# Kernel tuning notes

Hardware: AMD Instinct MI355X
Metric: run time of the kernel (lower is better)

## Reference

```python
import jax, jax.numpy as jnp
import numpy as np


def setup_inputs() -> dict:
    key = jax.random.key(0)
    k1, k2, k3 = jax.random.split(key, 3)
    Bt, N, Fin, Fout = 16, 4096, 1024, 1024
    X = jax.random.normal(k1, (Bt, N, Fin), dtype=jnp.float32)
    B = jax.random.normal(k2, (Fin, Fout), dtype=jnp.float32) * (1.0 / np.sqrt(Fin))
    cT = jax.random.normal(k3, (1, Fout), dtype=jnp.float32) * (1.0 / np.sqrt(Fin))
    return {"X": X, "B": B, "cT": cT}


def reference(X, B, cT):
    # Original computes (1/N) * (o1 @ o1.T) @ X @ B + o1 @ cT,
    # which is mathematically mean(X, axis=-2) @ B + cT broadcast to all N rows.
    N = X.shape[-2]
    mean = jnp.mean(X, axis=-2, keepdims=True)          # [..., 1, Fin]
    row = mean @ B + cT                                  # [..., 1, Fout]
    return jnp.broadcast_to(row, X.shape[:-1] + (B.shape[1],))
```

## Files before the change

kernel.cpp:

```cpp
#include <hip/hip_runtime.h>

#define BT   16
#define NR   4096
#define FIN  1024
#define FOUT 1024

#define NCHUNK 32
#define ROWS_PER_CHUNK (NR / NCHUNK)
#define ROWS_PER_BLOCK 32

__global__ void colsum_partial(const float* __restrict__ X, float* __restrict__ part) {
    const int rc = blockIdx.x;
    const int b  = blockIdx.y;
    const int t  = threadIdx.x;
    const float4* src = reinterpret_cast<const float4*>(
        X + (size_t)b * NR * FIN + (size_t)rc * ROWS_PER_CHUNK * FIN) + t;
    float4 acc = {0.f, 0.f, 0.f, 0.f};
#pragma unroll 8
    for (int r = 0; r < ROWS_PER_CHUNK; ++r) {
        float4 v = src[(size_t)r * (FIN / 4)];
        acc.x += v.x; acc.y += v.y; acc.z += v.z; acc.w += v.w;
    }
    reinterpret_cast<float4*>(part + ((size_t)b * NCHUNK + rc) * FIN)[t] = acc;
}

__global__ void colsum_finish(const float* __restrict__ part, float* __restrict__ mean) {
    const int b = blockIdx.x;
    const int t = threadIdx.x;
    const float4* src = reinterpret_cast<const float4*>(part + (size_t)b * NCHUNK * FIN) + t;
    float4 acc = {0.f, 0.f, 0.f, 0.f};
#pragma unroll
    for (int c = 0; c < NCHUNK; ++c) {
        float4 v = src[(size_t)c * (FIN / 4)];
        acc.x += v.x; acc.y += v.y; acc.z += v.z; acc.w += v.w;
    }
    const float inv = 1.0f / (float)NR;
    acc.x *= inv; acc.y *= inv; acc.z *= inv; acc.w *= inv;
    reinterpret_cast<float4*>(mean + (size_t)b * FIN)[t] = acc;
}

__global__ void matvec_row(const float* __restrict__ mean, const float* __restrict__ Bm,
                           const float* __restrict__ cT, float* __restrict__ row) {
    const int foc = blockIdx.x;
    const int b   = blockIdx.y;
    const int t   = threadIdx.x;
    const int fo  = foc * 256 + t;
    __shared__ float sm[FIN];
    for (int i = t; i < FIN; i += 256) sm[i] = mean[(size_t)b * FIN + i];
    __syncthreads();
    float acc = cT[fo];
#pragma unroll 8
    for (int fi = 0; fi < FIN; ++fi) {
        acc += sm[fi] * Bm[(size_t)fi * FOUT + fo];
    }
    row[(size_t)b * FOUT + fo] = acc;
}

__global__ void bcast_rows(const float* __restrict__ row, float* __restrict__ out) {
    const int rc = blockIdx.x;
    const int b  = blockIdx.y;
    const int t  = threadIdx.x;
    const float4 v = reinterpret_cast<const float4*>(row + (size_t)b * FOUT)[t];
    float4* dst = reinterpret_cast<float4*>(
        out + (size_t)b * NR * FOUT + (size_t)rc * ROWS_PER_BLOCK * FOUT) + t;
#pragma unroll 8
    for (int r = 0; r < ROWS_PER_BLOCK; ++r) {
        dst[(size_t)r * (FOUT / 4)] = v;
    }
}

extern "C" void kernel_launch(void* const* d_in, const int* in_sizes, int n_in,
                              void* d_out, int out_size, void* d_ws, size_t ws_size,
                              hipStream_t stream) {
    const float* X  = (const float*)d_in[0];
    const float* Bm = (const float*)d_in[1];
    const float* cT = (const float*)d_in[2];
    float* out = (float*)d_out;

    float* part = (float*)d_ws;
    float* mean = part + (size_t)BT * NCHUNK * FIN;
    float* row  = mean + (size_t)BT * FIN;

    colsum_partial<<<dim3(NCHUNK, BT), 256, 0, stream>>>(X, part);
    colsum_finish<<<dim3(BT), 256, 0, stream>>>(part, mean);
    matvec_row<<<dim3(FOUT / 256, BT), 256, 0, stream>>>(mean, Bm, cT, row);
    bcast_rows<<<dim3(NR / ROWS_PER_BLOCK, BT), 256, 0, stream>>>(row, out);
}
```

Before: 518.2 us.

## Fuse colsum finish into matvec and split matvec reduction across thread groups

Doubles the number of row chunks in the partial column-sum to raise parallelism, and uses two independent accumulators there. The separate finish kernel is folded into the matvec, where each block redundantly reduces the partials into shared memory. The matvec now gives 64 outputs per block, splits the Fin dimension over four thread groups and reduces them in shared memory, so it launches more blocks. This removes one launch and raises occupancy, at the cost of re-reading the partials in every matvec block.

```diff
diff --git a/kernel.cpp b/kernel.cpp
--- a/kernel.cpp
+++ b/kernel.cpp
@@ -5,7 +5,7 @@
 #define FIN  1024
 #define FOUT 1024
 
-#define NCHUNK 32
+#define NCHUNK 64
 #define ROWS_PER_CHUNK (NR / NCHUNK)
 #define ROWS_PER_BLOCK 32
 
@@ -15,45 +15,54 @@
     const int t  = threadIdx.x;
     const float4* src = reinterpret_cast<const float4*>(
         X + (size_t)b * NR * FIN + (size_t)rc * ROWS_PER_CHUNK * FIN) + t;
-    float4 acc = {0.f, 0.f, 0.f, 0.f};
-#pragma unroll 8
-    for (int r = 0; r < ROWS_PER_CHUNK; ++r) {
-        float4 v = src[(size_t)r * (FIN / 4)];
-        acc.x += v.x; acc.y += v.y; acc.z += v.z; acc.w += v.w;
+    float4 a0 = {0.f, 0.f, 0.f, 0.f};
+    float4 a1 = {0.f, 0.f, 0.f, 0.f};
+#pragma unroll 4
+    for (int r = 0; r < ROWS_PER_CHUNK; r += 2) {
+        float4 v0 = src[(size_t)r       * (FIN / 4)];
+        float4 v1 = src[(size_t)(r + 1) * (FIN / 4)];
+        a0.x += v0.x; a0.y += v0.y; a0.z += v0.z; a0.w += v0.w;
+        a1.x += v1.x; a1.y += v1.y; a1.z += v1.z; a1.w += v1.w;
     }
+    float4 acc = {a0.x + a1.x, a0.y + a1.y, a0.z + a1.z, a0.w + a1.w};
     reinterpret_cast<float4*>(part + ((size_t)b * NCHUNK + rc) * FIN)[t] = acc;
 }
 
-__global__ void colsum_finish(const float* __restrict__ part, float* __restrict__ mean) {
-    const int b = blockIdx.x;
-    const int t = threadIdx.x;
-    const float4* src = reinterpret_cast<const float4*>(part + (size_t)b * NCHUNK * FIN) + t;
-    float4 acc = {0.f, 0.f, 0.f, 0.f};
-#pragma unroll
-    for (int c = 0; c < NCHUNK; ++c) {
-        float4 v = src[(size_t)c * (FIN / 4)];
-        acc.x += v.x; acc.y += v.y; acc.z += v.z; acc.w += v.w;
-    }
-    const float inv = 1.0f / (float)NR;
-    acc.x *= inv; acc.y *= inv; acc.z *= inv; acc.w *= inv;
-    reinterpret_cast<float4*>(mean + (size_t)b * FIN)[t] = acc;
-}
-
-__global__ void matvec_row(const float* __restrict__ mean, const float* __restrict__ Bm,
-                           const float* __restrict__ cT, float* __restrict__ row) {
+__global__ void matvec_fused(const float* __restrict__ part, const float* __restrict__ Bm,
+                             const float* __restrict__ cT, float* __restrict__ row) {
     const int foc = blockIdx.x;
     const int b   = blockIdx.y;
     const int t   = threadIdx.x;
-    const int fo  = foc * 256 + t;
     __shared__ float sm[FIN];
-    for (int i = t; i < FIN; i += 256) sm[i] = mean[(size_t)b * FIN + i];
+    __shared__ float red[4][64];
+    {
+        const float4* src = reinterpret_cast<const float4*>(part + (size_t)b * NCHUNK * FIN) + t;
+        float4 a = {0.f, 0.f, 0.f, 0.f};
+#pragma unroll 8
+        for (int c = 0; c < NCHUNK; ++c) {
+            float4 v = src[(size_t)c * (FIN / 4)];
+            a.x += v.x; a.y += v.y; a.z += v.z; a.w += v.w;
+        }
+        const float inv = 1.0f / (float)NR;
+        reinterpret_cast<float4*>(sm)[t] = make_float4(a.x * inv, a.y * inv, a.z * inv, a.w * inv);
+    }
     __syncthreads();
-    float acc = cT[fo];
+    const int fo_idx = t & 63;
+    const int g      = t >> 6;
+    const int fo     = foc * 64 + fo_idx;
+    const float* bp  = Bm + (size_t)(g * 256) * FOUT + fo;
+    float f0 = 0.f, f1 = 0.f;
 #pragma unroll 8
-    for (int fi = 0; fi < FIN; ++fi) {
-        acc += sm[fi] * Bm[(size_t)fi * FOUT + fo];
+    for (int k = 0; k < 256; k += 2) {
+        f0 += sm[g * 256 + k]     * bp[(size_t)k       * FOUT];
+        f1 += sm[g * 256 + k + 1] * bp[(size_t)(k + 1) * FOUT];
     }
-    row[(size_t)b * FOUT + fo] = acc;
+    red[g][fo_idx] = f0 + f1;
+    __syncthreads();
+    if (g == 0) {
+        float r = red[0][fo_idx] + red[1][fo_idx] + red[2][fo_idx] + red[3][fo_idx] + cT[fo];
+        row[(size_t)b * FOUT + fo] = r;
+    }
 }
 
 __global__ void bcast_rows(const float* __restrict__ row, float* __restrict__ out) {
@@ -78,11 +87,9 @@
     float* out = (float*)d_out;
 
     float* part = (float*)d_ws;
-    float* mean = part + (size_t)BT * NCHUNK * FIN;
-    float* row  = mean + (size_t)BT * FIN;
+    float* row  = part + (size_t)BT * NCHUNK * FIN;
 
     colsum_partial<<<dim3(NCHUNK, BT), 256, 0, stream>>>(X, part);
-    colsum_finish<<<dim3(BT), 256, 0, stream>>>(part, mean);
-    matvec_row<<<dim3(FOUT / 256, BT), 256, 0, stream>>>(mean, Bm, cT, row);
+    matvec_fused<<<dim3(FOUT / 64, BT), 256, 0, stream>>>(part, Bm, cT, row);
     bcast_rows<<<dim3(NR / ROWS_PER_BLOCK, BT), 256, 0, stream>>>(row, out);
 }
```

New measurement: 467.0 us. 1.11x faster.

## Fuse colsum, matvec and broadcast into one cooperative persistent kernel

Applied to the files above, without the earlier changes.

Replaces four kernel launches with a single cooperative kernel of 1024 blocks that uses grid-wide syncs between the column-sum, mat-vec and broadcast phases. It falls back to three separate launches if the cooperative launch fails. The colsum work is redistributed so each block strides over the whole batch with two accumulators, and the partial reduction is folded into the mat-vec phase, where 16 blocks each compute four outputs per thread. This removes launch gaps and the separate finish kernel. In exchange, only 16 blocks do the mat-vec while the rest sit idle at a grid barrier.

```diff
diff --git a/kernel.cpp b/kernel.cpp
--- a/kernel.cpp
+++ b/kernel.cpp
@@ -1,72 +1,116 @@
 #include <hip/hip_runtime.h>
+#include <hip/hip_cooperative_groups.h>
+
+namespace cg = cooperative_groups;
 
 #define BT   16
 #define NR   4096
 #define FIN  1024
 #define FOUT 1024
 
-#define NCHUNK 32
-#define ROWS_PER_CHUNK (NR / NCHUNK)
-#define ROWS_PER_BLOCK 32
+#define BLOCKS 1024
+#define TPB    256
+#define BPB    (BLOCKS / BT)
+#define WPB    (BPB * TPB)
+#define NSLICE (WPB / (FIN / 4))
+#define STEPS  ((NR * FIN / 4) / WPB)
 
-__global__ void colsum_partial(const float* __restrict__ X, float* __restrict__ part) {
-    const int rc = blockIdx.x;
-    const int b  = blockIdx.y;
-    const int t  = threadIdx.x;
-    const float4* src = reinterpret_cast<const float4*>(
-        X + (size_t)b * NR * FIN + (size_t)rc * ROWS_PER_CHUNK * FIN) + t;
-    float4 acc = {0.f, 0.f, 0.f, 0.f};
+typedef float f32x4 __attribute__((ext_vector_type(4)));
+
+
+__device__ __forceinline__ void phase1_colsum(const float* __restrict__ X,
+                                              float* __restrict__ part,
+                                              int b, int w) {
+    const f32x4* src = reinterpret_cast<const f32x4*>(X + (size_t)b * NR * FIN) + w;
+    f32x4 a0 = {0.f, 0.f, 0.f, 0.f};
+    f32x4 a1 = {0.f, 0.f, 0.f, 0.f};
 #pragma unroll 8
-    for (int r = 0; r < ROWS_PER_CHUNK; ++r) {
-        float4 v = src[(size_t)r * (FIN / 4)];
-        acc.x += v.x; acc.y += v.y; acc.z += v.z; acc.w += v.w;
+    for (int k = 0; k < STEPS; k += 2) {
+        a0 += src[(size_t)k * WPB];
+        a1 += src[(size_t)(k + 1) * WPB];
     }
-    reinterpret_cast<float4*>(part + ((size_t)b * NCHUNK + rc) * FIN)[t] = acc;
+    f32x4 acc = a0 + a1;
+    reinterpret_cast<f32x4*>(part)[((size_t)b * NSLICE + (w >> 8)) * (FIN / 4) + (w & 255)] = acc;
 }
 
-__global__ void colsum_finish(const float* __restrict__ part, float* __restrict__ mean) {
-    const int b = blockIdx.x;
-    const int t = threadIdx.x;
-    const float4* src = reinterpret_cast<const float4*>(part + (size_t)b * NCHUNK * FIN) + t;
-    float4 acc = {0.f, 0.f, 0.f, 0.f};
-#pragma unroll
-    for (int c = 0; c < NCHUNK; ++c) {
-        float4 v = src[(size_t)c * (FIN / 4)];
-        acc.x += v.x; acc.y += v.y; acc.z += v.z; acc.w += v.w;
+__device__ __forceinline__ void phase2_matvec(const float* __restrict__ part,
+                                              const float* __restrict__ Bm,
+                                              const float* __restrict__ cT,
+                                              float* __restrict__ row,
+                                              int mb, int t, float* sm) {
+    const f32x4* ps = reinterpret_cast<const f32x4*>(part) + (size_t)mb * NSLICE * (FIN / 4) + t;
+    f32x4 a = {0.f, 0.f, 0.f, 0.f};
+#pragma unroll 8
+    for (int s = 0; s < NSLICE; ++s) a += ps[(size_t)s * (FIN / 4)];
+    a *= (1.0f / (float)NR);
+    reinterpret_cast<f32x4*>(sm)[t] = a;
+    __syncthreads();
+    float acc0 = cT[t], acc1 = cT[t + 256], acc2 = cT[t + 512], acc3 = cT[t + 768];
+#pragma unroll 4
+    for (int fi = 0; fi < FIN; ++fi) {
+        const float m = sm[fi];
+        const float* bp = Bm + (size_t)fi * FOUT + t;
+        acc0 += m * bp[0];
+        acc1 += m * bp[256];
+        acc2 += m * bp[512];
+        acc3 += m * bp[768];
     }
-    const float inv = 1.0f / (float)NR;
-    acc.x *= inv; acc.y *= inv; acc.z *= inv; acc.w *= inv;
-    reinterpret_cast<float4*>(mean + (size_t)b * FIN)[t] = acc;
+    float* rp = row + (size_t)mb * FOUT + t;
+    rp[0] = acc0; rp[256] = acc1; rp[512] = acc2; rp[768] = acc3;
 }
 
-__global__ void matvec_row(const float* __restrict__ mean, const float* __restrict__ Bm,
-                           const float* __restrict__ cT, float* __restrict__ row) {
-    const int foc = blockIdx.x;
-    const int b   = blockIdx.y;
-    const int t   = threadIdx.x;
-    const int fo  = foc * 256 + t;
-    __shared__ float sm[FIN];
-    for (int i = t; i < FIN; i += 256) sm[i] = mean[(size_t)b * FIN + i];
-    __syncthreads();
-    float acc = cT[fo];
+__device__ __forceinline__ void phase3_bcast(const float* __restrict__ row,
+                                             float* __restrict__ out,
+                                             int b, int w) {
+    const f32x4 v = reinterpret_cast<const f32x4*>(row + (size_t)b * FOUT)[w & 255];
+    f32x4* dst = reinterpret_cast<f32x4*>(out + (size_t)b * NR * FOUT) + w;
 #pragma unroll 8
-    for (int fi = 0; fi < FIN; ++fi) {
-        acc += sm[fi] * Bm[(size_t)fi * FOUT + fo];
+    for (int k = 0; k < STEPS; ++k) {
+        dst[(size_t)k * WPB] = v;
     }
-    row[(size_t)b * FOUT + fo] = acc;
 }
 
-__global__ void bcast_rows(const float* __restrict__ row, float* __restrict__ out) {
-    const int rc = blockIdx.x;
-    const int b  = blockIdx.y;
-    const int t  = threadIdx.x;
-    const float4 v = reinterpret_cast<const float4*>(row + (size_t)b * FOUT)[t];
-    float4* dst = reinterpret_cast<float4*>(
-        out + (size_t)b * NR * FOUT + (size_t)rc * ROWS_PER_BLOCK * FOUT) + t;
-#pragma unroll 8
-    for (int r = 0; r < ROWS_PER_BLOCK; ++r) {
-        dst[(size_t)r * (FOUT / 4)] = v;
+__global__ __launch_bounds__(TPB, 4) void fused_all(
+        const float* __restrict__ X, const float* __restrict__ Bm,
+        const float* __restrict__ cT, float* __restrict__ part,
+        float* __restrict__ row, float* __restrict__ out) {
+    cg::grid_group grid = cg::this_grid();
+    const int b = blockIdx.x >> 6;
+    const int w = ((blockIdx.x & (BPB - 1)) << 8) | threadIdx.x;
+    const int t = threadIdx.x;
+
+    phase1_colsum(X, part, b, w);
+    __threadfence();
+    grid.sync();
+
+    if (blockIdx.x < BT) {
+        __shared__ float sm[FIN];
+        phase2_matvec(part, Bm, cT, row, blockIdx.x, t, sm);
     }
+    __threadfence();
+    grid.sync();
+
+    phase3_bcast(row, out, b, w);
+}
+
+__global__ __launch_bounds__(TPB) void k_colsum(const float* __restrict__ X,
+                                                float* __restrict__ part) {
+    const int b = blockIdx.x >> 6;
+    const int w = ((blockIdx.x & (BPB - 1)) << 8) | threadIdx.x;
+    phase1_colsum(X, part, b, w);
+}
+__global__ __launch_bounds__(TPB) void k_matvec(const float* __restrict__ part,
+                                                const float* __restrict__ Bm,
+                                                const float* __restrict__ cT,
+                                                float* __restrict__ row) {
+    __shared__ float sm[FIN];
+    phase2_matvec(part, Bm, cT, row, blockIdx.x, threadIdx.x, sm);
+}
+__global__ __launch_bounds__(TPB) void k_bcast(const float* __restrict__ row,
+                                               float* __restrict__ out) {
+    const int b = blockIdx.x >> 6;
+    const int w = ((blockIdx.x & (BPB - 1)) << 8) | threadIdx.x;
+    phase3_bcast(row, out, b, w);
 }
 
 extern "C" void kernel_launch(void* const* d_in, const int* in_sizes, int n_in,
@@ -78,11 +122,14 @@
     float* out = (float*)d_out;
 
     float* part = (float*)d_ws;
-    float* mean = part + (size_t)BT * NCHUNK * FIN;
-    float* row  = mean + (size_t)BT * FIN;
+    float* row  = part + (size_t)BT * NSLICE * FIN;
 
-    colsum_partial<<<dim3(NCHUNK, BT), 256, 0, stream>>>(X, part);
-    colsum_finish<<<dim3(BT), 256, 0, stream>>>(part, mean);
-    matvec_row<<<dim3(FOUT / 256, BT), 256, 0, stream>>>(mean, Bm, cT, row);
-    bcast_rows<<<dim3(NR / ROWS_PER_BLOCK, BT), 256, 0, stream>>>(row, out);
+    void* args[] = {(void*)&X, (void*)&Bm, (void*)&cT, (void*)&part, (void*)&row, (void*)&out};
+    hipError_t err = hipLaunchCooperativeKernel((void*)fused_all, dim3(BLOCKS), dim3(TPB),
+                                                args, 0, stream);
+    if (err != hipSuccess) {
+        k_colsum<<<dim3(BLOCKS), TPB, 0, stream>>>(X, part);
+        k_matvec<<<dim3(BT), TPB, 0, stream>>>(part, Bm, cT, row);
+        k_bcast<<<dim3(BLOCKS), TPB, 0, stream>>>(row, out);
+    }
 }
```

After: 1.027 ms. 98.2% more time.
